# Kernel tuning notes

Measured on AMD Instinct MI355X. Metric: run time of the kernel, lower is better.

## Reference

```python
import jax, jax.numpy as jnp
import numpy as np

B, P, L = 32, 256, 32            # samples, max paths/sample, tokens/path
V, DE, DP = 30000, 256, 256      # vocab, node emb dim, path emb dim
NH, DH = 8, 32                   # heads, head dim (NH*DH == DP)
DFF = 1024
NLAYERS = 4
MAXCHILD = 32
NEG = -1e9


def setup_inputs() -> dict:
    key = jax.random.key(0)
    ks = jax.random.split(key, 32)
    s = 0.02
    inp = {}
    inp['tokens'] = jax.random.randint(ks[0], (B, P, L), 0, V, dtype=jnp.int32)
    inp['paths_count'] = jax.random.randint(ks[1], (B,), 2, P + 1, dtype=jnp.int32)
    inp['target_indices'] = jax.random.randint(ks[2], (B,), 0, MAXCHILD, dtype=jnp.int32)
    inp['emb'] = jax.random.normal(ks[3], (V, DE)) * s
    inp['lstm1_k'] = jax.random.normal(ks[4], (DE, 4 * DP)) * s
    inp['lstm1_r'] = jax.random.normal(ks[5], (DP, 4 * DP)) * s
    inp['lstm1_b'] = jnp.zeros((4 * DP,))
    inp['lstm2_k'] = jax.random.normal(ks[6], (DP, 4 * DP)) * s
    inp['lstm2_r'] = jax.random.normal(ks[7], (DP, 4 * DP)) * s
    inp['lstm2_b'] = jnp.zeros((4 * DP,))
    inp['enc_wq'] = jax.random.normal(ks[8], (NLAYERS, DP, DP)) * s
    inp['enc_wk'] = jax.random.normal(ks[9], (NLAYERS, DP, DP)) * s
    inp['enc_wv'] = jax.random.normal(ks[10], (NLAYERS, DP, DP)) * s
    inp['enc_wo'] = jax.random.normal(ks[11], (NLAYERS, DP, DP)) * s
    inp['enc_ln1_g'] = jnp.ones((NLAYERS, DP))
    inp['enc_ln1_b'] = jnp.zeros((NLAYERS, DP))
    inp['enc_w1'] = jax.random.normal(ks[12], (NLAYERS, DP, DFF)) * s
    inp['enc_b1'] = jnp.zeros((NLAYERS, DFF))
    inp['enc_w2'] = jax.random.normal(ks[13], (NLAYERS, DFF, DP)) * s
    inp['enc_b2'] = jnp.zeros((NLAYERS, DP))
    inp['enc_ln2_g'] = jnp.ones((NLAYERS, DP))
    inp['enc_ln2_b'] = jnp.zeros((NLAYERS, DP))
    inp['W_r'] = jax.random.normal(ks[14], (DP, DP)) * s
    inp['W_g'] = jax.random.normal(ks[15], (2 * DP, DE)) * s
    inp['C_i'] = jax.random.normal(ks[16], (MAXCHILD, DP, DP)) * s
    return inp


def _lstm(x, K, R, b, return_seq):
    """Keras-style LSTM (gate order i,f,g,o). x: [N, L, d]."""
    N = x.shape[0]
    u = R.shape[0]
    def step(carry, xt):
        h, c = carry
        z = xt @ K + h @ R + b
        i, f, g, o = jnp.split(z, 4, axis=-1)
        c = jax.nn.sigmoid(f) * c + jax.nn.sigmoid(i) * jnp.tanh(g)
        h = jax.nn.sigmoid(o) * jnp.tanh(c)
        return (h, c), (h if return_seq else 0.0)
    init = (jnp.zeros((N, u), x.dtype), jnp.zeros((N, u), x.dtype))
    (h_last, _), ys = jax.lax.scan(step, init, jnp.swapaxes(x, 0, 1))
    return jnp.swapaxes(ys, 0, 1) if return_seq else h_last


def _layernorm(x, g, b):
    m = jnp.mean(x, axis=-1, keepdims=True)
    v = jnp.mean(jnp.square(x - m), axis=-1, keepdims=True)
    return (x - m) * jax.lax.rsqrt(v + 1e-5) * g + b


def _encoder_layer(x, mask, wq, wk, wv, wo, g1, bb1, w1, b1, w2, b2, g2, bb2):
    Bs, n, d = x.shape
    q = (x @ wq).reshape(Bs, n, NH, DH)
    k = (x @ wk).reshape(Bs, n, NH, DH)
    v = (x @ wv).reshape(Bs, n, NH, DH)
    scores = jnp.einsum('bqhd,bkhd->bhqk', q, k) / np.sqrt(DH).astype(np.float32)
    scores = jnp.where(mask[:, None, :, :], scores, NEG)
    a = jax.nn.softmax(scores, axis=-1)
    o = jnp.einsum('bhqk,bkhd->bqhd', a, v).reshape(Bs, n, d) @ wo
    x = _layernorm(x + o, g1, bb1)
    f = jax.nn.relu(x @ w1 + b1) @ w2 + b2
    return _layernorm(x + f, g2, bb2)


def reference(tokens, paths_count, target_indices, emb,
              lstm1_k, lstm1_r, lstm1_b, lstm2_k, lstm2_r, lstm2_b,
              enc_wq, enc_wk, enc_wv, enc_wo, enc_ln1_g, enc_ln1_b,
              enc_w1, enc_b1, enc_w2, enc_b2, enc_ln2_g, enc_ln2_b,
              W_r, W_g, C_i):
    # embed + ragged->flat paths: [B*P, L, DE]
    e = emb[tokens].reshape(B * P, L, DE)
    h1 = _lstm(e, lstm1_k, lstm1_r, lstm1_b, return_seq=True)      # [B*P, L, DP]
    h2 = _lstm(h1, lstm2_k, lstm2_r, lstm2_b, return_seq=False)    # [B*P, DP]
    Hall = h2.reshape(B, P, DP)

    # last valid path per sample is the root context R
    R = Hall[jnp.arange(B), paths_count - 1]                        # [B, DP]
    n = P - 1
    valid = jnp.arange(n)[None, :] < (paths_count - 1)[:, None]     # [B, n]
    H = jnp.where(valid[:, :, None], Hall[:, :n, :], 0.0)           # padded dense, zeros like to_tensor
    mask = valid[:, :, None] & valid[:, None, :]                    # per-sample block mask

    Z = H
    for l in range(NLAYERS):
        Z = _encoder_layer(Z, mask, enc_wq[l], enc_wk[l], enc_wv[l], enc_wo[l],
                           enc_ln1_g[l], enc_ln1_b[l], enc_w1[l], enc_b1[l],
                           enc_w2[l], enc_b2[l], enc_ln2_g[l], enc_ln2_b[l])

    # per-sample transform matrix gather and attention pooling
    C = C_i[target_indices]                                         # [B, DP, DP]
    R = jnp.einsum('bij,bj->bi', C, R)
    R = jax.nn.relu(R) @ W_r                                        # [B, DP]
    alpha = jax.nn.softmax(jnp.einsum('bnd,bd->bn', Z, R), axis=-1) # note: no pad mask (faithful)
    Zp = jnp.einsum('bn,bnd->bd', alpha, Z)                         # [B, DP]
    h = jax.nn.relu(jnp.concatenate([Zp, R], axis=-1) @ W_g)        # [B, DE]
    return jax.nn.softmax(h @ emb.T, axis=-1)                       # [B, V]
```

## Files before the change

kernel.cpp:

```cpp
#include <hip/hip_runtime.h>
#include <cstdint>
#include <cstddef>

typedef unsigned short u16;
typedef unsigned int   u32;
typedef float f32x4 __attribute__((ext_vector_type(4)));
typedef short s16x8 __attribute__((ext_vector_type(8)));
typedef u32   u32x4 __attribute__((ext_vector_type(4)));

#define DEV static __device__ __forceinline__


static constexpr size_t OFF_EMBB = 0;
static constexpr size_t OFF_WP1  = 15360000;
static constexpr size_t OFF_WP2  = 16408576;
static constexpr size_t OFF_BQKV = 17457152;
static constexpr size_t OFF_WOT  = 19030016;
static constexpr size_t OFF_W1ET = 19554304;
static constexpr size_t OFF_W2ET = 21651456;
static constexpr size_t OFF_CIT  = 23748608;
static constexpr size_t OFF_HALL = 32137216;
static constexpr size_t OFF_X    = 40525824;
static constexpr size_t OFF_XB   = 48914432;
static constexpr size_t OFF_Y    = 53108736;
static constexpr size_t OFF_QKV  = 61497344;
static constexpr size_t OFF_AO   = 74080256;
static constexpr size_t OFF_F    = 78274560;
static constexpr size_t OFF_RV   = 95051776;
static constexpr size_t OFF_HB   = 95084544;
static constexpr size_t OFF_LOG  = 95100928;
static constexpr size_t OFF_H1A  = OFF_X;
static constexpr size_t OFF_H1B  = OFF_X + 4194304;
static constexpr size_t OFF_H2A  = OFF_X + 8388608;
static constexpr size_t OFF_H2B  = OFF_X + 12582912;
static constexpr size_t OFF_BARC = OFF_X + 16777216;

DEV u16 f2bf(float f){ u32 u = __builtin_bit_cast(u32, f); u += 0x7fffu + ((u>>16)&1u); return (u16)(u>>16); }
DEV float bf2f(u16 v){ return __builtin_bit_cast(float, (u32)v<<16); }
DEV float sigm(float x){ return 1.f/(1.f+__expf(-x)); }
DEV float tanh_f(float x){ float e=__expf(-2.f*fabsf(x)); float t=(1.f-e)/(1.f+e); return x<0.f? -t:t; }
DEV f32x4 splat4(float x){ f32x4 v={x,x,x,x}; return v; }
DEV f32x4 mfma16(s16x8 a, s16x8 b, f32x4 c){ return __builtin_amdgcn_mfma_f32_16x16x32_bf16(a,b,c,0,0,0); }

DEV int swz256(int row, int col){ int ch=col>>3; return row*256 + (((ch ^ (row&7))&31)<<3) + (col&7); }
DEV int swz128(int row, int col){ int ch=col>>3; return row*128 + (((ch ^ (row&7))&15)<<3) + (col&7); }
DEV int swz32 (int row, int col){ int ch=col>>3; return row*32  + (((ch ^ (row&3))&3)<<3)  + (col&7); }

DEV void st32_s(u32* p, u32 v){
  asm volatile("global_store_dword %0, %1, off sc0 sc1" :: "v"(p), "v"(v) : "memory");
}
DEV u32 ld32_s(const u32* p){
  u32 r;
  asm volatile("global_load_dword %0, %1, off sc0 sc1\n\ts_waitcnt vmcnt(0)" : "=v"(r) : "v"(p) : "memory");
  return r;
}
DEV u32x4 ld128_s(const u32* p){
  u32x4 r;
  asm volatile("global_load_dwordx4 %0, %1, off sc0 sc1\n\ts_waitcnt vmcnt(0)" : "=v"(r) : "v"(p) : "memory");
  return r;
}
DEV void st16_s(u16* p, u16 v){
  asm volatile("global_store_short %0, %1, off sc0 sc1" :: "v"(p), "v"((u32)v) : "memory");
}
template<bool FAST>
DEV void ld8(const u16* pa, const u16* pb, s16x8 r[8]){
  if constexpr (FAST){
    asm volatile(
      "global_load_dwordx4 %0, %8, off sc0\n\t"
      "global_load_dwordx4 %1, %8, off offset:64 sc0\n\t"
      "global_load_dwordx4 %2, %8, off offset:128 sc0\n\t"
      "global_load_dwordx4 %3, %8, off offset:192 sc0\n\t"
      "global_load_dwordx4 %4, %9, off sc0\n\t"
      "global_load_dwordx4 %5, %9, off offset:64 sc0\n\t"
      "global_load_dwordx4 %6, %9, off offset:128 sc0\n\t"
      "global_load_dwordx4 %7, %9, off offset:192 sc0\n\t"
      "s_waitcnt vmcnt(0)"
      : "=&v"(r[0]),"=&v"(r[1]),"=&v"(r[2]),"=&v"(r[3]),
        "=&v"(r[4]),"=&v"(r[5]),"=&v"(r[6]),"=&v"(r[7])
      : "v"(pa), "v"(pb) : "memory");
  } else {
    asm volatile(
      "global_load_dwordx4 %0, %8, off sc0 sc1\n\t"
      "global_load_dwordx4 %1, %8, off offset:64 sc0 sc1\n\t"
      "global_load_dwordx4 %2, %8, off offset:128 sc0 sc1\n\t"
      "global_load_dwordx4 %3, %8, off offset:192 sc0 sc1\n\t"
      "global_load_dwordx4 %4, %9, off sc0 sc1\n\t"
      "global_load_dwordx4 %5, %9, off offset:64 sc0 sc1\n\t"
      "global_load_dwordx4 %6, %9, off offset:128 sc0 sc1\n\t"
      "global_load_dwordx4 %7, %9, off offset:192 sc0 sc1\n\t"
      "s_waitcnt vmcnt(0)"
      : "=&v"(r[0]),"=&v"(r[1]),"=&v"(r[2]),"=&v"(r[3]),
        "=&v"(r[4]),"=&v"(r[5]),"=&v"(r[6]),"=&v"(r[7])
      : "v"(pa), "v"(pb) : "memory");
  }
}

DEV void gbar(u32* arr, u32 gen){
  __syncthreads();
  if (threadIdx.x==0){
    asm volatile("s_waitcnt vmcnt(0)" ::: "memory");
    st32_s(arr + blockIdx.x, gen);
  }
  if (threadIdx.x < 64){
    bool done = false;
    do {
      u32x4 q = ld128_s(arr + threadIdx.x*4);
      done = __all(q.x>=gen && q.y>=gen && q.z>=gen && q.w>=gen);
      if (!done) __builtin_amdgcn_s_sleep(8);
    } while(!done);
  }
  __syncthreads();
}

struct TJob { const float* src; u32 dstOff; int K; int N; int stride; int f32out; };
struct PrepArgs { TJob j[60]; };

__global__ void k_prep(PrepArgs pa, char* __restrict__ ws){
  TJob jb = pa.j[blockIdx.y];
  int tilesK = jb.K >> 5, tilesN = jb.N >> 5;
  int ti = blockIdx.x;
  if (ti >= tilesK*tilesN) return;
  int tk = ti % tilesK, tn = ti / tilesK;
  __shared__ float tile[32][33];
  int r = threadIdx.x >> 5, c = threadIdx.x & 31;
  #pragma unroll
  for (int rr=0; rr<32; rr+=8)
    tile[rr+r][c] = jb.src[(size_t)(tk*32+rr+r)*jb.N + tn*32 + c];
  __syncthreads();
  if (jb.f32out){
    float* dst = (float*)(ws + jb.dstOff);
    #pragma unroll
    for (int rr=0; rr<32; rr+=8)
      dst[(size_t)(tn*32+rr+r)*jb.stride + tk*32 + c] = tile[c][rr+r];
  } else {
    u16* dst = (u16*)(ws + jb.dstOff);
    #pragma unroll
    for (int rr=0; rr<32; rr+=8)
      dst[(size_t)(tn*32+rr+r)*jb.stride + tk*32 + c] = f2bf(tile[c][rr+r]);
  }
}

__global__ void k_embcvt(const float* __restrict__ src, u16* __restrict__ dst, int n4){
  int i = blockIdx.x*blockDim.x + threadIdx.x;
  if (i >= n4) return;
  float4 v = ((const float4*)src)[i];
  uint2 pk;
  pk.x = f2bf(v.x) | ((u32)f2bf(v.y)<<16);
  pk.y = f2bf(v.z) | ((u32)f2bf(v.w)<<16);
  ((uint2*)dst)[i] = pk;
}

__global__ void k_packfrag(const float* __restrict__ srcA, const float* __restrict__ srcB,
                           u16* __restrict__ dst)
{
  int gid = blockIdx.x*256 + threadIdx.x;
  int lane = gid & 63;
  int hs   = (gid>>6) & 15;
  int c    = gid >> 10;
  int kc = c>>2, g = c&3;
  int l4 = lane>>4, l15 = lane&15;
  int col = g*256 + hs*16 + l15;
  int k0  = kc*32 + l4*8;
  u16 out[8];
  #pragma unroll
  for (int j=0;j<8;++j){
    int k = k0 + j;
    float v = (k < 256) ? srcA[(size_t)k*1024 + col] : srcB[(size_t)(k-256)*1024 + col];
    out[j] = f2bf(v);
  }
  *(s16x8*)(dst + (size_t)gid*8) = *(const s16x8*)out;
}

template<bool FAST>
DEV void lstm_steps(const int* __restrict__ tokens, const u16* __restrict__ EMBB,
    const u16* W1s, const u16* W2s, int* tokl,
    const float bl1[4], const float bl2[4],
    u16* H1A, u16* H1B, u16* H2A, u16* H2B,
    u32* arr, float* __restrict__ Hall,
    int tid, int lane, int v, int l15, int l4, int sg, int hs, int seq0w, u32 gen)
{
  float c1[8], c2[8];
  #pragma unroll
  for (int i=0;i<8;++i){ c1[i]=0.f; c2[i]=0.f; }
  #pragma unroll 1
  for (int t=0;t<32;++t){
    const u16* H1r = (t&1)? H1B : H1A;  u16* H1w = (t&1)? H1A : H1B;
    const u16* H2r = (t&1)? H2B : H2A;  u16* H2w = (t&1)? H2A : H2B;
    if (tid < 512) tokl[tid] = tokens[(sg*512 + tid)*32 + t];
    __syncthreads();
    const int tok0 = tokl[v*32 + l15], tok1 = tokl[v*32 + 16 + l15];
    f32x4 acc[2][4];
    #pragma unroll
    for (int g=0;g<4;++g){ acc[0][g]=splat4(bl1[g]); acc[1][g]=splat4(bl1[g]); }
    #pragma unroll
    for (int kc=0;kc<8;++kc){
      s16x8 fa0 = *(const s16x8*)(EMBB + (size_t)tok0*256 + kc*32 + l4*8);
      s16x8 fa1 = *(const s16x8*)(EMBB + (size_t)tok1*256 + kc*32 + l4*8);
      #pragma unroll
      for (int g=0;g<4;++g){
        s16x8 wf = *(const s16x8*)&W1s[(kc*4+g)*512 + lane*8];
        acc[0][g]=mfma16(fa0,wf,acc[0][g]);
        acc[1][g]=mfma16(fa1,wf,acc[1][g]);
      }
    }
    #pragma unroll
    for (int blk=0;blk<2;++blk){
      s16x8 r[8];
      ld8<FAST>(H1r + (size_t)(seq0w+l15)*256 + blk*128 + l4*8,
                H1r + (size_t)(seq0w+16+l15)*256 + blk*128 + l4*8, r);
      #pragma unroll
      for (int k2=0;k2<4;++k2){
        int kc = 8 + blk*4 + k2;
        #pragma unroll
        for (int g=0;g<4;++g){
          s16x8 wf = *(const s16x8*)&W1s[(kc*4+g)*512 + lane*8];
          acc[0][g]=mfma16(r[k2],wf,acc[0][g]);
          acc[1][g]=mfma16(r[4+k2],wf,acc[1][g]);
        }
      }
    }
    #pragma unroll
    for (int m=0;m<2;++m)
      #pragma unroll
      for (int rr=0;rr<4;++rr){
        int idx=m*4+rr;
        float zi=acc[m][0][rr], zf=acc[m][1][rr], zg=acc[m][2][rr], zo=acc[m][3][rr];
        float cc=sigm(zf)*c1[idx]+sigm(zi)*tanh_f(zg);
        c1[idx]=cc;
        u16 hb=f2bf(sigm(zo)*tanh_f(cc));
        u16* p = H1w + (size_t)(seq0w + m*16 + l4*4 + rr)*256 + hs*16 + l15;
        if constexpr (FAST) *p = hb; else st16_s(p, hb);
      }
    ++gen; gbar(arr, gen);
    #pragma unroll
    for (int g=0;g<4;++g){ acc[0][g]=splat4(bl2[g]); acc[1][g]=splat4(bl2[g]); }
    #pragma unroll
    for (int blk=0;blk<2;++blk){
      s16x8 r[8];
      ld8<FAST>(H1w + (size_t)(seq0w+l15)*256 + blk*128 + l4*8,
                H1w + (size_t)(seq0w+16+l15)*256 + blk*128 + l4*8, r);
      #pragma unroll
      for (int k2=0;k2<4;++k2){
        int kc = blk*4 + k2;
        #pragma unroll
        for (int g=0;g<4;++g){
          s16x8 wf = *(const s16x8*)&W2s[(kc*4+g)*512 + lane*8];
          acc[0][g]=mfma16(r[k2],wf,acc[0][g]);
          acc[1][g]=mfma16(r[4+k2],wf,acc[1][g]);
        }
      }
    }
    #pragma unroll
    for (int blk=0;blk<2;++blk){
      s16x8 r[8];
      ld8<FAST>(H2r + (size_t)(seq0w+l15)*256 + blk*128 + l4*8,
                H2r + (size_t)(seq0w+16+l15)*256 + blk*128 + l4*8, r);
      #pragma unroll
      for (int k2=0;k2<4;++k2){
        int kc = 8 + blk*4 + k2;
        #pragma unroll
        for (int g=0;g<4;++g){
          s16x8 wf = *(const s16x8*)&W2s[(kc*4+g)*512 + lane*8];
          acc[0][g]=mfma16(r[k2],wf,acc[0][g]);
          acc[1][g]=mfma16(r[4+k2],wf,acc[1][g]);
        }
      }
    }
    #pragma unroll
    for (int m=0;m<2;++m)
      #pragma unroll
      for (int rr=0;rr<4;++rr){
        int idx=m*4+rr;
        float zi=acc[m][0][rr], zf=acc[m][1][rr], zg=acc[m][2][rr], zo=acc[m][3][rr];
        float cc=sigm(zf)*c2[idx]+sigm(zi)*tanh_f(zg);
        c2[idx]=cc;
        float h=sigm(zo)*tanh_f(cc);
        u16 hb=f2bf(h);
        u16* p = H2w + (size_t)(seq0w + m*16 + l4*4 + rr)*256 + hs*16 + l15;
        if constexpr (FAST) *p = hb; else st16_s(p, hb);
        if (t==31) Hall[(size_t)(seq0w + m*16 + l4*4 + rr)*256 + hs*16 + l15] = h;
      }
    ++gen; gbar(arr, gen);
  }
}

__global__ __launch_bounds__(1024,4) void k_lstm3(
    const int* __restrict__ tokens, const u16* __restrict__ EMBB,
    const u16* __restrict__ WP1, const u16* __restrict__ WP2,
    const float* __restrict__ b1, const float* __restrict__ b2,
    u16* __restrict__ H1A, u16* __restrict__ H1B,
    u16* __restrict__ H2A, u16* __restrict__ H2B,
    u32* __restrict__ bar, float* __restrict__ Hall)
{
  __shared__ u16 W1s[64*512];
  __shared__ u16 W2s[64*512];
  __shared__ int tokl[512];
  __shared__ int fastf;
  const int tid=threadIdx.x, lane=tid&63, v=tid>>6, l15=lane&15, l4=lane>>4;
  const int bid=blockIdx.x, sg=bid&15, hs=bid>>4;
  const int seq0w = sg*512 + v*32;
  u32* arr    = bar;
  u32* xcctab = bar + 256;

  #pragma unroll
  for (int i=0;i<4;++i){
    int c = v*4+i;
    const u16* s1 = WP1 + ((size_t)(c*16+hs))*512 + lane*8;
    const u16* s2 = WP2 + ((size_t)(c*16+hs))*512 + lane*8;
    __builtin_amdgcn_global_load_lds((const __attribute__((address_space(1))) void*)s1,
        (__attribute__((address_space(3))) void*)(W1s + c*512), 16, 0, 0);
    __builtin_amdgcn_global_load_lds((const __attribute__((address_space(1))) void*)s2,
        (__attribute__((address_space(3))) void*)(W2s + c*512), 16, 0, 0);
  }
  float bl1[4], bl2[4];
  #pragma unroll
  for (int g=0;g<4;++g){ bl1[g]=b1[g*256 + hs*16 + l15]; bl2[g]=b2[g*256 + hs*16 + l15]; }
  asm volatile("s_waitcnt vmcnt(0)" ::: "memory");
  __syncthreads();

  u32 myxcc = (__builtin_amdgcn_s_getreg((31<<11)|20) & 0xffu) | 0x100u;
  if (tid==0) st32_s(xcctab + bid, myxcc);
  gbar(arr, 1);
  if (v==0){
    bool sib_ok = true;
    if (lane < 16){
      u32 o = ld32_s(xcctab + (sg + 16*lane));
      sib_ok = (o == myxcc);
    }
    bool sibs = __all(sib_ok);
    u32x4 q = ld128_s(xcctab + lane*4);
    u32 ref = __shfl((int)q.x, 0, 64);
    bool allsame = __all(q.x==ref && q.y==ref && q.z==ref && q.w==ref);
    if (lane==0) fastf = (sibs && !allsame) ? 1 : 0;
  }
  __syncthreads();

  if (fastf) lstm_steps<true >(tokens, EMBB, W1s, W2s, tokl, bl1, bl2, H1A,H1B,H2A,H2B, arr, Hall,
                               tid, lane, v, l15, l4, sg, hs, seq0w, 1u);
  else       lstm_steps<false>(tokens, EMBB, W1s, W2s, tokl, bl1, bl2, H1A,H1B,H2A,H2B, arr, Hall,
                               tid, lane, v, l15, l4, sg, hs, seq0w, 1u);
}

template<int BM, int EPI>
__global__ __launch_bounds__(512,2) void k_gemm(
    const u16* __restrict__ A, const u16* __restrict__ Bt, void* __restrict__ Cv,
    const float* __restrict__ bias, const float* __restrict__ Res,
    int M, int N, int K, int ldC)
{
  __shared__ u16 Asl[BM*256];
  const int tid=threadIdx.x, lane=tid&63, w=tid>>6, l15=lane&15, l4=lane>>4;
  const int mb=blockIdx.x, nb=blockIdx.y;
  constexpr int MT = BM/16;
  const int col0 = nb*256 + w*32;
  float bz0=0.f, bz1=0.f;
  if (EPI==1 || EPI==3 || EPI==5){ bz0 = bias[col0 + l15]; bz1 = bias[col0 + 16 + l15]; }
  f32x4 acc[MT][2];
  #pragma unroll
  for (int mt=0;mt<MT;++mt){ acc[mt][0]=splat4(bz0); acc[mt][1]=splat4(bz1); }
  for (int kb=0; kb<K; kb+=256){
    __syncthreads();
    if (tid < BM*8){
      int row=tid>>3, part=tid&7;
      int arow = mb*BM+row; if (arow > M-1) arow = M-1;
      const u16* src = A + (size_t)arow*K + kb + part*32;
      #pragma unroll
      for (int i=0;i<4;++i)
        *(s16x8*)&Asl[swz256(row, part*32+i*8)] = *(const s16x8*)(src+i*8);
    }
    __syncthreads();
    #pragma unroll
    for (int kc=0; kc<8; ++kc){
      s16x8 fa[MT];
      #pragma unroll
      for (int mt=0;mt<MT;++mt)
        fa[mt] = *(const s16x8*)&Asl[swz256(mt*16+l15, kc*32 + l4*8)];
      #pragma unroll
      for (int n=0;n<2;++n){
        int brow = col0 + n*16 + l15; if (brow > N-1) brow = N-1;
        const s16x8 fb = *(const s16x8*)(Bt + (size_t)brow*K + kb + kc*32 + l4*8);
        #pragma unroll
        for (int mt=0;mt<MT;++mt) acc[mt][n] = mfma16(fa[mt], fb, acc[mt][n]);
      }
    }
  }
  #pragma unroll
  for (int mt=0;mt<MT;++mt){
    #pragma unroll
    for (int n=0;n<2;++n){
      #pragma unroll
      for (int r=0;r<4;++r){
        int row = mb*BM + mt*16 + l4*4 + r;
        int col = col0 + n*16 + l15;
        if (col < N && row < M){
          float v = acc[mt][n][r];
          if (EPI==0){ ((u16*)Cv)[(size_t)row*ldC + col] = f2bf(v); }
          else if (EPI==1){ ((u16*)Cv)[(size_t)row*ldC + col] = f2bf(fmaxf(v,0.f)); }
          else if (EPI==2 || EPI==3){ ((float*)Cv)[(size_t)row*ldC + col] = v + Res[(size_t)row*ldC + col]; }
          else if (EPI==5){ ((u16*)Cv)[(size_t)row*ldC + col] = f2bf(v); }
          else { ((float*)Cv)[(size_t)row*ldC + col] = v; }
        }
      }
    }
  }
}

__global__ __launch_bounds__(256) void k_attn(const u16* __restrict__ QKV, u16* __restrict__ AO,
                                              const int* __restrict__ pc)
{
  __shared__ u16 Qs[256*32];
  __shared__ u16 Ks[256*32];
  __shared__ u16 Vt[32*256];
  __shared__ u16 Ab[4][64*128];
  const int bh=blockIdx.x, b=bh>>3, h=bh&7;
  const int tid=threadIdx.x, lane=tid&63, w=tid>>6, l15=lane&15, l4=lane>>4;
  const int pcm1 = pc[b]-1;
  {
    int row = tid;
    const u16* base = QKV + (size_t)(b*256+row)*768 + h*32;
    #pragma unroll
    for (int i=0;i<4;++i){
      *(s16x8*)&Qs[swz32(row, i*8)] = *(const s16x8*)(base + i*8);
      *(s16x8*)&Ks[swz32(row, i*8)] = *(const s16x8*)(base + 256 + i*8);
    }
    #pragma unroll
    for (int i=0;i<4;++i){
      s16x8 v = *(const s16x8*)(base + 512 + i*8);
      #pragma unroll
      for (int j=0;j<8;++j){
        int d = i*8+j;
        Vt[d*256 + ((((row>>3) ^ (d&7))&31)<<3) + (row&7)] = (u16)v[j];
      }
    }
  }
  __syncthreads();
  const float scale = 0.17677669529663689f;
  const int q0w = w*64;
  float rmax[4][4], rinv[4][4];
  #pragma unroll 1
  for (int m=0;m<4;++m){
    f32x4 sacc[16];
    #pragma unroll
    for (int nt=0;nt<16;++nt) sacc[nt]=splat4(0.f);
    s16x8 fa = *(const s16x8*)&Qs[swz32(q0w+m*16+l15, l4*8)];
    #pragma unroll
    for (int nt=0;nt<16;++nt){
      s16x8 fb = *(const s16x8*)&Ks[swz32(nt*16+l15, l4*8)];
      sacc[nt] = mfma16(fa, fb, sacc[nt]);
    }
    #pragma unroll
    for (int r=0;r<4;++r){
      int q = q0w + m*16 + l4*4 + r;
      bool vq = q < pcm1;
      float sv[16]; float mx = -3e38f;
      #pragma unroll
      for (int nt=0;nt<16;++nt){
        int k = nt*16 + l15;
        float s = (vq && k < pcm1) ? sacc[nt][r]*scale : -1e9f;
        if (k == 255) s = -1e30f;
        sv[nt] = s; mx = fmaxf(mx, s);
      }
      #pragma unroll
      for (int msk=1;msk<16;msk<<=1) mx = fmaxf(mx, __shfl_xor(mx, msk, 64));
      float sum = 0.f;
      #pragma unroll
      for (int nt=0;nt<16;++nt) sum += __expf(sv[nt]-mx);
      #pragma unroll
      for (int msk=1;msk<16;msk<<=1) sum += __shfl_xor(sum, msk, 64);
      rmax[m][r]=mx; rinv[m][r]=1.f/sum;
    }
  }
  f32x4 oacc[4][2];
  #pragma unroll
  for (int m=0;m<4;++m){ oacc[m][0]=splat4(0.f); oacc[m][1]=splat4(0.f); }
  #pragma unroll 1
  for (int kg=0; kg<2; ++kg){
    #pragma unroll 1
    for (int m=0;m<4;++m){
      s16x8 fa = *(const s16x8*)&Qs[swz32(q0w+m*16+l15, l4*8)];
      #pragma unroll
      for (int nt2=0;nt2<8;++nt2){
        int nt = kg*8 + nt2;
        s16x8 fb = *(const s16x8*)&Ks[swz32(nt*16+l15, l4*8)];
        f32x4 sa = mfma16(fa, fb, splat4(0.f));
        #pragma unroll
        for (int r=0;r<4;++r){
          int q = q0w + m*16 + l4*4 + r;
          int k = nt*16 + l15;
          float s = (q < pcm1 && k < pcm1) ? sa[r]*scale : -1e9f;
          if (k == 255) s = -1e30f;
          float p = __expf(s - rmax[m][r]) * rinv[m][r];
          Ab[w][swz128(m*16 + l4*4 + r, nt2*16 + l15)] = f2bf(p);
        }
      }
    }
    #pragma unroll 1
    for (int m=0;m<4;++m){
      #pragma unroll
      for (int kc=0;kc<4;++kc){
        s16x8 fa2 = *(const s16x8*)&Ab[w][swz128(m*16+l15, kc*32 + l4*8)];
        #pragma unroll
        for (int n=0;n<2;++n){
          int d = n*16 + l15;
          int kch = kg*16 + kc*4 + l4;
          s16x8 fb = *(const s16x8*)&Vt[d*256 + (((kch ^ (d&7))&31)<<3)];
          oacc[m][n] = mfma16(fa2, fb, oacc[m][n]);
        }
      }
    }
  }
  #pragma unroll
  for (int m=0;m<4;++m){
    #pragma unroll
    for (int n=0;n<2;++n){
      #pragma unroll
      for (int r=0;r<4;++r){
        int q = q0w + m*16 + l4*4 + r;
        AO[(size_t)(b*256+q)*256 + h*32 + n*16 + l15] = f2bf(oacc[m][n][r]);
      }
    }
  }
}

__global__ void k_ln(const float* __restrict__ Y, const float* __restrict__ g, const float* __restrict__ bb,
                     float* __restrict__ X, u16* __restrict__ Xb)
{
  int w = threadIdx.x >> 6, lane = threadIdx.x & 63;
  int row = blockIdx.x*4 + w;
  float4 v = ((const float4*)(Y + (size_t)row*256))[lane];
  float s = v.x+v.y+v.z+v.w;
  #pragma unroll
  for (int m=1;m<64;m<<=1) s += __shfl_xor(s, m, 64);
  float mean = s * (1.f/256.f);
  float dx=v.x-mean, dy=v.y-mean, dz=v.z-mean, dw=v.w-mean;
  float q = dx*dx+dy*dy+dz*dz+dw*dw;
  #pragma unroll
  for (int m=1;m<64;m<<=1) q += __shfl_xor(q, m, 64);
  float rstd = rsqrtf(q*(1.f/256.f) + 1e-5f);
  int c = lane*4;
  float o0=dx*rstd*g[c]+bb[c], o1=dy*rstd*g[c+1]+bb[c+1], o2=dz*rstd*g[c+2]+bb[c+2], o3=dw*rstd*g[c+3]+bb[c+3];
  float4 o; o.x=o0; o.y=o1; o.z=o2; o.w=o3;
  ((float4*)(X + (size_t)row*256))[lane] = o;
  uint2 pk; pk.x = f2bf(o0) | ((u32)f2bf(o1)<<16); pk.y = f2bf(o2) | ((u32)f2bf(o3)<<16);
  ((uint2*)(Xb + (size_t)row*256))[lane] = pk;
}

__global__ void k_buildZ(const float* __restrict__ Hall, const int* __restrict__ pc,
                         float* __restrict__ X, u16* __restrict__ Xb)
{
  int gid = blockIdx.x*256 + threadIdx.x;
  int row = gid >> 6;
  int b = row >> 8, p = row & 255;
  float4 v; v.x=v.y=v.z=v.w=0.f;
  if (p < pc[b]-1) v = ((const float4*)Hall)[gid];
  ((float4*)X)[gid] = v;
  uint2 pk; pk.x = f2bf(v.x) | ((u32)f2bf(v.y)<<16); pk.y = f2bf(v.z) | ((u32)f2bf(v.w)<<16);
  ((uint2*)Xb)[gid] = pk;
}

__global__ void k_rprep(const float* __restrict__ Hall, const int* __restrict__ pc, const int* __restrict__ tgt,
                        const float* __restrict__ CIT, const float* __restrict__ Wr, float* __restrict__ RV)
{
  int b = blockIdx.x, t = threadIdx.x;
  __shared__ float r0[256], ys[256];
  r0[t] = Hall[(size_t)(b*256 + pc[b]-1)*256 + t];
  __syncthreads();
  const float* Cb = CIT + (size_t)tgt[b]*65536;
  float a = 0.f;
  for (int j=0;j<256;++j) a += Cb[j*256 + t] * r0[j];
  ys[t] = fmaxf(a, 0.f);
  __syncthreads();
  float a2 = 0.f;
  for (int i=0;i<256;++i) a2 += Wr[i*256 + t] * ys[i];
  RV[b*256 + t] = a2;
}

__global__ void k_pool(const float* __restrict__ X, const float* __restrict__ RV,
                       const float* __restrict__ Wg, u16* __restrict__ HB)
{
  int b = blockIdx.x, t = threadIdx.x;
  __shared__ float R[256], al[256], red[256], zp[256];
  R[t] = RV[b*256+t];
  __syncthreads();
  float sc = -3e38f;
  if (t < 255){
    const float* z = X + (size_t)(b*256+t)*256;
    float a=0.f;
    for (int d=0;d<256;++d) a += z[d]*R[d];
    sc = a;
  }
  red[t] = sc;
  __syncthreads();
  for (int s=128;s>0;s>>=1){ if (t<s) red[t]=fmaxf(red[t],red[t+s]); __syncthreads(); }
  float M = red[0];
  __syncthreads();
  float e = (t<255) ? __expf(sc - M) : 0.f;
  red[t] = e;
  __syncthreads();
  for (int s=128;s>0;s>>=1){ if (t<s) red[t]+=red[t+s]; __syncthreads(); }
  float S = red[0];
  al[t] = e / S;
  __syncthreads();
  float acc = 0.f;
  for (int p=0;p<255;++p) acc += al[p] * X[(size_t)(b*256+p)*256 + t];
  zp[t] = acc;
  __syncthreads();
  float a2 = 0.f;
  for (int d=0;d<256;++d) a2 += zp[d] * Wg[d*256 + t];
  for (int d=0;d<256;++d) a2 += R[d]  * Wg[(256+d)*256 + t];
  HB[b*256+t] = f2bf(fmaxf(a2, 0.f));
}

__global__ void k_osm(const float* __restrict__ LOG, float* __restrict__ out)
{
  int b = blockIdx.x, t = threadIdx.x;
  __shared__ float red[512];
  const float* Lp = LOG + (size_t)b*30000;
  float mx = -3e38f;
  for (int i=t;i<30000;i+=512) mx = fmaxf(mx, Lp[i]);
  red[t]=mx; __syncthreads();
  for (int s=256;s>0;s>>=1){ if (t<s) red[t]=fmaxf(red[t],red[t+s]); __syncthreads(); }
  float M = red[0]; __syncthreads();
  float sm = 0.f;
  for (int i=t;i<30000;i+=512) sm += __expf(Lp[i]-M);
  red[t]=sm; __syncthreads();
  for (int s=256;s>0;s>>=1){ if (t<s) red[t]+=red[t+s]; __syncthreads(); }
  float rinv = 1.f/red[0];
  float* O = out + (size_t)b*30000;
  for (int i=t;i<30000;i+=512) O[i] = __expf(Lp[i]-M) * rinv;
}

extern "C" void kernel_launch(void* const* d_in, const int* in_sizes, int n_in,
                              void* d_out, int out_size, void* d_ws, size_t ws_size,
                              hipStream_t stream)
{
  const int*   tokens = (const int*)  d_in[0];
  const int*   pc     = (const int*)  d_in[1];
  const int*   tgt    = (const int*)  d_in[2];
  const float* emb    = (const float*)d_in[3];
  const float* l1k    = (const float*)d_in[4];
  const float* l1r    = (const float*)d_in[5];
  const float* l1b    = (const float*)d_in[6];
  const float* l2k    = (const float*)d_in[7];
  const float* l2r    = (const float*)d_in[8];
  const float* l2b    = (const float*)d_in[9];
  const float* wq     = (const float*)d_in[10];
  const float* wk     = (const float*)d_in[11];
  const float* wv     = (const float*)d_in[12];
  const float* wo     = (const float*)d_in[13];
  const float* ln1g   = (const float*)d_in[14];
  const float* ln1b   = (const float*)d_in[15];
  const float* w1e    = (const float*)d_in[16];
  const float* b1e    = (const float*)d_in[17];
  const float* w2e    = (const float*)d_in[18];
  const float* b2e    = (const float*)d_in[19];
  const float* ln2g   = (const float*)d_in[20];
  const float* ln2b   = (const float*)d_in[21];
  const float* Wr     = (const float*)d_in[22];
  const float* Wg     = (const float*)d_in[23];
  const float* Ci     = (const float*)d_in[24];

  char* ws = (char*)d_ws;
  u16*   EMBB = (u16*)  (ws + OFF_EMBB);
  u16*   WP1  = (u16*)  (ws + OFF_WP1);
  u16*   WP2  = (u16*)  (ws + OFF_WP2);
  float* CIT  = (float*)(ws + OFF_CIT);
  float* HALL = (float*)(ws + OFF_HALL);
  float* X    = (float*)(ws + OFF_X);
  u16*   XB   = (u16*)  (ws + OFF_XB);
  float* Y    = (float*)(ws + OFF_Y);
  u16*   QKVb = (u16*)  (ws + OFF_QKV);
  u16*   AOb  = (u16*)  (ws + OFF_AO);
  u16*   Fb   = (u16*)  (ws + OFF_F);
  float* RV   = (float*)(ws + OFF_RV);
  u16*   HB   = (u16*)  (ws + OFF_HB);
  float* LOGp = (float*)(ws + OFF_LOG);
  u16*   H1A  = (u16*)  (ws + OFF_H1A);
  u16*   H1B  = (u16*)  (ws + OFF_H1B);
  u16*   H2A  = (u16*)  (ws + OFF_H2A);
  u16*   H2B  = (u16*)  (ws + OFF_H2B);
  u32*   BARC = (u32*)  (ws + OFF_BARC);

  PrepArgs pa;
  int ji = 0;
  auto addJ = [&](const float* s, size_t off, int K, int N, int stride, int f32o){
    pa.j[ji].src=s; pa.j[ji].dstOff=(u32)off; pa.j[ji].K=K; pa.j[ji].N=N; pa.j[ji].stride=stride; pa.j[ji].f32out=f32o; ++ji;
  };
  for (int l=0;l<4;++l) addJ(wq + l*65536,  OFF_BQKV + (size_t)(l*768      )*512, 256,256,256,0);
  for (int l=0;l<4;++l) addJ(wk + l*65536,  OFF_BQKV + (size_t)(l*768 + 256)*512, 256,256,256,0);
  for (int l=0;l<4;++l) addJ(wv + l*65536,  OFF_BQKV + (size_t)(l*768 + 512)*512, 256,256,256,0);
  for (int l=0;l<4;++l) addJ(wo + l*65536,  OFF_WOT  + (size_t)l*131072, 256,256,256,0);
  for (int l=0;l<4;++l) addJ(w1e + l*262144, OFF_W1ET + (size_t)l*524288, 256,1024,256,0);
  for (int l=0;l<4;++l) addJ(w2e + l*262144, OFF_W2ET + (size_t)l*524288, 1024,256,1024,0);
  for (int c=0;c<32;++c) addJ(Ci + (size_t)c*65536, OFF_CIT + (size_t)c*262144, 256,256,256,1);

  hipMemsetAsync(ws + OFF_H1A, 0, 16777216 + 2048, stream);
  k_prep<<<dim3(256,56), dim3(256), 0, stream>>>(pa, ws);
  k_embcvt<<<dim3(7500), dim3(256), 0, stream>>>(emb, EMBB, 1920000);
  k_packfrag<<<dim3(256), dim3(256), 0, stream>>>(l1k, l1r, WP1);
  k_packfrag<<<dim3(256), dim3(256), 0, stream>>>(l2k, l2r, WP2);
  k_lstm3<<<dim3(256), dim3(1024), 0, stream>>>(tokens, EMBB, WP1, WP2, l1b, l2b,
                                                H1A, H1B, H2A, H2B, BARC, HALL);
  k_buildZ<<<dim3(2048), dim3(256), 0, stream>>>(HALL, pc, X, XB);
  k_rprep<<<dim3(32), dim3(256), 0, stream>>>(HALL, pc, tgt, CIT, Wr, RV);

  u16* BQKV = (u16*)(ws + OFF_BQKV);
  u16* WOT  = (u16*)(ws + OFF_WOT);
  u16* W1ET = (u16*)(ws + OFF_W1ET);
  u16* W2ET = (u16*)(ws + OFF_W2ET);
  for (int l=0;l<4;++l){
    k_gemm<64,0><<<dim3(128,3), dim3(512), 0, stream>>>(XB, BQKV + (size_t)l*768*256, QKVb, nullptr, nullptr, 8192, 768, 256, 768);
    k_attn<<<dim3(256), dim3(256), 0, stream>>>(QKVb, AOb, pc);
    k_gemm<64,2><<<dim3(128,1), dim3(512), 0, stream>>>(AOb, WOT + (size_t)l*65536, Y, nullptr, X, 8192, 256, 256, 256);
    k_ln<<<dim3(2048), dim3(256), 0, stream>>>(Y, ln1g + l*256, ln1b + l*256, X, XB);
    k_gemm<64,1><<<dim3(128,4), dim3(512), 0, stream>>>(XB, W1ET + (size_t)l*262144, Fb, b1e + l*1024, nullptr, 8192, 1024, 256, 1024);
    k_gemm<64,3><<<dim3(128,1), dim3(512), 0, stream>>>(Fb, W2ET + (size_t)l*262144, Y, b2e + l*256, X, 8192, 256, 1024, 256);
    k_ln<<<dim3(2048), dim3(256), 0, stream>>>(Y, ln2g + l*256, ln2b + l*256, X, XB);
  }

  k_pool<<<dim3(32), dim3(256), 0, stream>>>(X, RV, Wg, HB);
  k_gemm<32,4><<<dim3(1,118), dim3(512), 0, stream>>>(HB, EMBB, LOGp, nullptr, nullptr, 32, 30000, 256, 30000);
  k_osm<<<dim3(32), dim3(512), 0, stream>>>(LOGp, (float*)d_out);
}
```

Baseline: 2.107 ms.

## Drop second grid barrier per LSTM step and prefetch hidden-state loads early

The LSTM step loop now uses one grid-wide barrier per timestep instead of two. The double-buffered H1/H2 ping-pong already orders the reads and writes, so the second barrier is redundant. The recurrent hidden-state loads are issued as one batch of 16 vector loads before the embedding MFMAs so their latency overlaps that compute. Tokens are read straight from global memory instead of being staged through LDS behind a __syncthreads, and the barrier spin sleep is shortened. The risk is subtle races if the buffer reasoning is wrong, plus more register pressure from the 16 in-flight vectors.

```diff
diff --git a/kernel.cpp b/kernel.cpp
--- a/kernel.cpp
+++ b/kernel.cpp
@@ -9,6 +9,7 @@
 typedef u32   u32x4 __attribute__((ext_vector_type(4)));
 
 #define DEV static __device__ __forceinline__
+#define WAIT0SB() do{ asm volatile("s_waitcnt vmcnt(0)" ::: "memory"); __builtin_amdgcn_sched_barrier(0); }while(0)
 
 
 static constexpr size_t OFF_EMBB = 0;
@@ -63,34 +64,52 @@
   asm volatile("global_store_short %0, %1, off sc0 sc1" :: "v"(p), "v"((u32)v) : "memory");
 }
 template<bool FAST>
-DEV void ld8(const u16* pa, const u16* pb, s16x8 r[8]){
+DEV void ld16_iss(const u16* pa, const u16* pb, s16x8 r[16]){
   if constexpr (FAST){
     asm volatile(
-      "global_load_dwordx4 %0, %8, off sc0\n\t"
-      "global_load_dwordx4 %1, %8, off offset:64 sc0\n\t"
-      "global_load_dwordx4 %2, %8, off offset:128 sc0\n\t"
-      "global_load_dwordx4 %3, %8, off offset:192 sc0\n\t"
-      "global_load_dwordx4 %4, %9, off sc0\n\t"
-      "global_load_dwordx4 %5, %9, off offset:64 sc0\n\t"
-      "global_load_dwordx4 %6, %9, off offset:128 sc0\n\t"
-      "global_load_dwordx4 %7, %9, off offset:192 sc0\n\t"
-      "s_waitcnt vmcnt(0)"
+      "global_load_dwordx4 %0, %16, off sc0\n\t"
+      "global_load_dwordx4 %1, %16, off offset:64 sc0\n\t"
+      "global_load_dwordx4 %2, %16, off offset:128 sc0\n\t"
+      "global_load_dwordx4 %3, %16, off offset:192 sc0\n\t"
+      "global_load_dwordx4 %4, %16, off offset:256 sc0\n\t"
+      "global_load_dwordx4 %5, %16, off offset:320 sc0\n\t"
+      "global_load_dwordx4 %6, %16, off offset:384 sc0\n\t"
+      "global_load_dwordx4 %7, %16, off offset:448 sc0\n\t"
+      "global_load_dwordx4 %8, %17, off sc0\n\t"
+      "global_load_dwordx4 %9, %17, off offset:64 sc0\n\t"
+      "global_load_dwordx4 %10, %17, off offset:128 sc0\n\t"
+      "global_load_dwordx4 %11, %17, off offset:192 sc0\n\t"
+      "global_load_dwordx4 %12, %17, off offset:256 sc0\n\t"
+      "global_load_dwordx4 %13, %17, off offset:320 sc0\n\t"
+      "global_load_dwordx4 %14, %17, off offset:384 sc0\n\t"
+      "global_load_dwordx4 %15, %17, off offset:448 sc0"
       : "=&v"(r[0]),"=&v"(r[1]),"=&v"(r[2]),"=&v"(r[3]),
-        "=&v"(r[4]),"=&v"(r[5]),"=&v"(r[6]),"=&v"(r[7])
+        "=&v"(r[4]),"=&v"(r[5]),"=&v"(r[6]),"=&v"(r[7]),
+        "=&v"(r[8]),"=&v"(r[9]),"=&v"(r[10]),"=&v"(r[11]),
+        "=&v"(r[12]),"=&v"(r[13]),"=&v"(r[14]),"=&v"(r[15])
       : "v"(pa), "v"(pb) : "memory");
   } else {
     asm volatile(
-      "global_load_dwordx4 %0, %8, off sc0 sc1\n\t"
-      "global_load_dwordx4 %1, %8, off offset:64 sc0 sc1\n\t"
-      "global_load_dwordx4 %2, %8, off offset:128 sc0 sc1\n\t"
-      "global_load_dwordx4 %3, %8, off offset:192 sc0 sc1\n\t"
-      "global_load_dwordx4 %4, %9, off sc0 sc1\n\t"
-      "global_load_dwordx4 %5, %9, off offset:64 sc0 sc1\n\t"
-      "global_load_dwordx4 %6, %9, off offset:128 sc0 sc1\n\t"
-      "global_load_dwordx4 %7, %9, off offset:192 sc0 sc1\n\t"
-      "s_waitcnt vmcnt(0)"
+      "global_load_dwordx4 %0, %16, off sc0 sc1\n\t"
+      "global_load_dwordx4 %1, %16, off offset:64 sc0 sc1\n\t"
+      "global_load_dwordx4 %2, %16, off offset:128 sc0 sc1\n\t"
+      "global_load_dwordx4 %3, %16, off offset:192 sc0 sc1\n\t"
+      "global_load_dwordx4 %4, %16, off offset:256 sc0 sc1\n\t"
+      "global_load_dwordx4 %5, %16, off offset:320 sc0 sc1\n\t"
+      "global_load_dwordx4 %6, %16, off offset:384 sc0 sc1\n\t"
+      "global_load_dwordx4 %7, %16, off offset:448 sc0 sc1\n\t"
+      "global_load_dwordx4 %8, %17, off sc0 sc1\n\t"
+      "global_load_dwordx4 %9, %17, off offset:64 sc0 sc1\n\t"
+      "global_load_dwordx4 %10, %17, off offset:128 sc0 sc1\n\t"
+      "global_load_dwordx4 %11, %17, off offset:192 sc0 sc1\n\t"
+      "global_load_dwordx4 %12, %17, off offset:256 sc0 sc1\n\t"
+      "global_load_dwordx4 %13, %17, off offset:320 sc0 sc1\n\t"
+      "global_load_dwordx4 %14, %17, off offset:384 sc0 sc1\n\t"
+      "global_load_dwordx4 %15, %17, off offset:448 sc0 sc1"
       : "=&v"(r[0]),"=&v"(r[1]),"=&v"(r[2]),"=&v"(r[3]),
-        "=&v"(r[4]),"=&v"(r[5]),"=&v"(r[6]),"=&v"(r[7])
+        "=&v"(r[4]),"=&v"(r[5]),"=&v"(r[6]),"=&v"(r[7]),
+        "=&v"(r[8]),"=&v"(r[9]),"=&v"(r[10]),"=&v"(r[11]),
+        "=&v"(r[12]),"=&v"(r[13]),"=&v"(r[14]),"=&v"(r[15])
       : "v"(pa), "v"(pb) : "memory");
   }
 }
@@ -106,7 +125,7 @@
     do {
       u32x4 q = ld128_s(arr + threadIdx.x*4);
       done = __all(q.x>=gen && q.y>=gen && q.z>=gen && q.w>=gen);
-      if (!done) __builtin_amdgcn_s_sleep(8);
+      if (!done) __builtin_amdgcn_s_sleep(2);
     } while(!done);
   }
   __syncthreads();
@@ -173,23 +192,24 @@
 
 template<bool FAST>
 DEV void lstm_steps(const int* __restrict__ tokens, const u16* __restrict__ EMBB,
-    const u16* W1s, const u16* W2s, int* tokl,
+    const u16* W1s, const u16* W2s,
     const float bl1[4], const float bl2[4],
     u16* H1A, u16* H1B, u16* H2A, u16* H2B,
     u32* arr, float* __restrict__ Hall,
-    int tid, int lane, int v, int l15, int l4, int sg, int hs, int seq0w, u32 gen)
+    int lane, int v, int l15, int l4, int sg, int hs, int seq0w, u32 gen)
 {
   float c1[8], c2[8];
   #pragma unroll
   for (int i=0;i<8;++i){ c1[i]=0.f; c2[i]=0.f; }
+  const int row0 = seq0w + l15, row1 = seq0w + 16 + l15;
   #pragma unroll 1
   for (int t=0;t<32;++t){
     const u16* H1r = (t&1)? H1B : H1A;  u16* H1w = (t&1)? H1A : H1B;
     const u16* H2r = (t&1)? H2B : H2A;  u16* H2w = (t&1)? H2A : H2B;
-    if (tid < 512) tokl[tid] = tokens[(sg*512 + tid)*32 + t];
-    __syncthreads();
-    const int tok0 = tokl[v*32 + l15], tok1 = tokl[v*32 + 16 + l15];
+    const int tok0 = tokens[row0*32 + t], tok1 = tokens[row1*32 + t];
     f32x4 acc[2][4];
+    s16x8 r[16];
+    ld16_iss<FAST>(H1r + (size_t)row0*256 + l4*8, H1r + (size_t)row1*256 + l4*8, r);
     #pragma unroll
     for (int g=0;g<4;++g){ acc[0][g]=splat4(bl1[g]); acc[1][g]=splat4(bl1[g]); }
     #pragma unroll
@@ -203,20 +223,14 @@
         acc[1][g]=mfma16(fa1,wf,acc[1][g]);
       }
     }
-    #pragma unroll
-    for (int blk=0;blk<2;++blk){
-      s16x8 r[8];
-      ld8<FAST>(H1r + (size_t)(seq0w+l15)*256 + blk*128 + l4*8,
-                H1r + (size_t)(seq0w+16+l15)*256 + blk*128 + l4*8, r);
-      #pragma unroll
-      for (int k2=0;k2<4;++k2){
-        int kc = 8 + blk*4 + k2;
-        #pragma unroll
-        for (int g=0;g<4;++g){
-          s16x8 wf = *(const s16x8*)&W1s[(kc*4+g)*512 + lane*8];
-          acc[0][g]=mfma16(r[k2],wf,acc[0][g]);
-          acc[1][g]=mfma16(r[4+k2],wf,acc[1][g]);
-        }
+    WAIT0SB();
+    #pragma unroll
+    for (int k2=0;k2<8;++k2){
+      #pragma unroll
+      for (int g=0;g<4;++g){
+        s16x8 wf = *(const s16x8*)&W1s[((8+k2)*4+g)*512 + lane*8];
+        acc[0][g]=mfma16(r[k2],wf,acc[0][g]);
+        acc[1][g]=mfma16(r[8+k2],wf,acc[1][g]);
       }
     }
     #pragma unroll
@@ -234,36 +248,26 @@
     ++gen; gbar(arr, gen);
     #pragma unroll
     for (int g=0;g<4;++g){ acc[0][g]=splat4(bl2[g]); acc[1][g]=splat4(bl2[g]); }
-    #pragma unroll
-    for (int blk=0;blk<2;++blk){
-      s16x8 r[8];
-      ld8<FAST>(H1w + (size_t)(seq0w+l15)*256 + blk*128 + l4*8,
-                H1w + (size_t)(seq0w+16+l15)*256 + blk*128 + l4*8, r);
-      #pragma unroll
-      for (int k2=0;k2<4;++k2){
-        int kc = blk*4 + k2;
-        #pragma unroll
-        for (int g=0;g<4;++g){
-          s16x8 wf = *(const s16x8*)&W2s[(kc*4+g)*512 + lane*8];
-          acc[0][g]=mfma16(r[k2],wf,acc[0][g]);
-          acc[1][g]=mfma16(r[4+k2],wf,acc[1][g]);
-        }
-      }
-    }
-    #pragma unroll
-    for (int blk=0;blk<2;++blk){
-      s16x8 r[8];
-      ld8<FAST>(H2r + (size_t)(seq0w+l15)*256 + blk*128 + l4*8,
-                H2r + (size_t)(seq0w+16+l15)*256 + blk*128 + l4*8, r);
-      #pragma unroll
-      for (int k2=0;k2<4;++k2){
-        int kc = 8 + blk*4 + k2;
-        #pragma unroll
-        for (int g=0;g<4;++g){
-          s16x8 wf = *(const s16x8*)&W2s[(kc*4+g)*512 + lane*8];
-          acc[0][g]=mfma16(r[k2],wf,acc[0][g]);
-          acc[1][g]=mfma16(r[4+k2],wf,acc[1][g]);
-        }
+    ld16_iss<FAST>(H1w + (size_t)row0*256 + l4*8, H1w + (size_t)row1*256 + l4*8, r);
+    WAIT0SB();
+    #pragma unroll
+    for (int k2=0;k2<8;++k2){
+      #pragma unroll
+      for (int g=0;g<4;++g){
+        s16x8 wf = *(const s16x8*)&W2s[(k2*4+g)*512 + lane*8];
+        acc[0][g]=mfma16(r[k2],wf,acc[0][g]);
+        acc[1][g]=mfma16(r[8+k2],wf,acc[1][g]);
+      }
+    }
+    ld16_iss<FAST>(H2r + (size_t)row0*256 + l4*8, H2r + (size_t)row1*256 + l4*8, r);
+    WAIT0SB();
+    #pragma unroll
+    for (int k2=0;k2<8;++k2){
+      #pragma unroll
+      for (int g=0;g<4;++g){
+        s16x8 wf = *(const s16x8*)&W2s[((8+k2)*4+g)*512 + lane*8];
+        acc[0][g]=mfma16(r[k2],wf,acc[0][g]);
+        acc[1][g]=mfma16(r[8+k2],wf,acc[1][g]);
       }
     }
     #pragma unroll
@@ -280,7 +284,6 @@
         if constexpr (FAST) *p = hb; else st16_s(p, hb);
         if (t==31) Hall[(size_t)(seq0w + m*16 + l4*4 + rr)*256 + hs*16 + l15] = h;
       }
-    ++gen; gbar(arr, gen);
   }
 }
 
@@ -294,7 +297,6 @@
 {
   __shared__ u16 W1s[64*512];
   __shared__ u16 W2s[64*512];
-  __shared__ int tokl[512];
   __shared__ int fastf;
   const int tid=threadIdx.x, lane=tid&63, v=tid>>6, l15=lane&15, l4=lane>>4;
   const int bid=blockIdx.x, sg=bid&15, hs=bid>>4;
@@ -335,10 +337,10 @@
   }
   __syncthreads();
 
-  if (fastf) lstm_steps<true >(tokens, EMBB, W1s, W2s, tokl, bl1, bl2, H1A,H1B,H2A,H2B, arr, Hall,
-                               tid, lane, v, l15, l4, sg, hs, seq0w, 1u);
-  else       lstm_steps<false>(tokens, EMBB, W1s, W2s, tokl, bl1, bl2, H1A,H1B,H2A,H2B, arr, Hall,
-                               tid, lane, v, l15, l4, sg, hs, seq0w, 1u);
+  if (fastf) lstm_steps<true >(tokens, EMBB, W1s, W2s, bl1, bl2, H1A,H1B,H2A,H2B, arr, Hall,
+                               lane, v, l15, l4, sg, hs, seq0w, 1u);
+  else       lstm_steps<false>(tokens, EMBB, W1s, W2s, bl1, bl2, H1A,H1B,H2A,H2B, arr, Hall,
+                               lane, v, l15, l4, sg, hs, seq0w, 1u);
 }
 
 template<int BM, int EPI>
```

Result: no change. 2.148 ms (+1.9%).
